# Kernel optimization log

Hardware: AMD Instinct MI355X
Metric: run time of the kernel (lower is better)

The kernel has to match this reference:

```python
import jax, jax.numpy as jnp
import numpy as np

OUTPUT_SIZE = 512


def _build_schedule(n, m):
    """Static pyramid-circuit schedule of Givens/RBS gates on n wires.

    Sequential gate order (matches theta ordering): for k = 1..n-1, apply
    gates on adjacent wire pairs (i, i+1) for i = k-1 down to max(k-m, 0).
    Total gates = (2n - m - 1) * m // 2. Gates are packed into a brickwork
    schedule (timestep t = 2(k-1) - i) so each layer touches disjoint pairs
    and the whole chain runs in T = n + m - 2 parallel layers.
    Padded slots point at dummy wires (n, n+1) and are masked to identity.
    """
    layers = {}
    t_idx = 0
    for k in range(1, n):
        for i in range(k - 1, max(k - m, 0) - 1, -1):
            t = 2 * (k - 1) - i
            layers.setdefault(t, []).append((i, t_idx))
            t_idx += 1
    T = max(layers) + 1
    W = max(len(v) for v in layers.values())
    wire = np.full((T, W), n, dtype=np.int32)   # pad gates hit dummy wires (n, n+1)
    tidx = np.zeros((T, W), dtype=np.int32)
    mask = np.zeros((T, W), dtype=np.float32)
    for t, gs in layers.items():
        for j, (i, ti) in enumerate(gs):
            wire[t, j] = i
            tidx[t, j] = ti
            mask[t, j] = 1.0
    return wire, tidx, mask


def apply_orthogonal(thetas, x, output_size):
    input_size = x.shape[-1]
    n, m = max(input_size, output_size), min(input_size, output_size)
    wire, tidx, mask = _build_schedule(n, m)
    if input_size < n:
        x = jnp.pad(x, ((0, 0), (0, n - input_size)))
    state = jnp.pad(x, ((0, 0), (0, 2)))          # two dummy columns for padded gate slots
    th = thetas[jnp.asarray(tidx)]                # [T, W]
    msk = jnp.asarray(mask)
    cos = jnp.where(msk > 0, jnp.cos(th), 1.0)    # padded slots -> identity rotation
    sin = jnp.where(msk > 0, jnp.sin(th), 0.0)
    wa = jnp.asarray(wire)                        # [T, W] first wire of each pair
    wb = wa + 1

    def step(st, layer):
        c, s, a_idx, b_idx = layer
        a = st[:, a_idx]                          # [B, W]
        b = st[:, b_idx]
        st = st.at[:, a_idx].set(c * a + s * b)   # RBS rotation on each pair
        st = st.at[:, b_idx].set(c * b - s * a)
        return st, None

    state, _ = jax.lax.scan(step, state, (cos, sin, wa, wb))
    return state[:, :output_size]


def setup_inputs():
    key = jax.random.key(0)
    k1, k2 = jax.random.split(key)
    B, N = 256, 512
    n_thetas = (2 * max(N, OUTPUT_SIZE) - min(N, OUTPUT_SIZE) - 1) * min(N, OUTPUT_SIZE) // 2
    x = jax.random.normal(k1, (B, N), dtype=jnp.float32)
    thetas = jax.random.uniform(k2, (n_thetas,), dtype=jnp.float32,
                                minval=-np.pi, maxval=np.pi)
    bias = jnp.zeros((OUTPUT_SIZE,), dtype=jnp.float32)
    return {"x": x, "thetas": thetas, "bias": bias}


def reference(x, thetas, bias):
    # normalize_inputs=False path; with_bias=True
    out = apply_orthogonal(thetas, x, OUTPUT_SIZE)
    return out + bias
```

## Files before the change

kernel.cpp:

```cpp
#include <hip/hip_runtime.h>
#include <stdint.h>


#define N_WIRES 512
#define BATCH   256
#define PAIRS   510
#define HALFP   255
#define PF      5
#define FINAL4  (PAIRS * 256)
#define TOTAL4  (FINAL4 + 128)
#define TOTAL2  (TOTAL4 * 2)

__global__ __launch_bounds__(256) void fused_kernel(
    const float* __restrict__ thetas, float2* __restrict__ W2) {
  int tid = blockIdx.x * 256 + threadIdx.x;
  if (tid >= TOTAL2) return;
  float c = 1.0f, s = 0.0f;
  if (tid < PAIRS * 512) {
    int p = tid >> 9, r = tid & 511;
    int q = r >> 7, L = (r >> 1) & 63, e = r & 1, h = q >> 1;
    int t = 2 * p + h;
    int i = 8 * L + 4 * (q & 1) + 2 * e + h;
    if (i <= min(t, 1020 - t)) {
      int k = ((t + i) >> 1) + 1;
      int idx = ((k * (k - 1)) >> 1) + (k - 1 - i);
      __sincosf(thetas[idx], &s, &c);
    }
    if (q == 3 && e == 1) c -= 1.0f;
  } else {
    int e = tid - PAIRS * 512;
    int L = e >> 2, j = e & 3;
    if (8 * L + 2 * j == 0) __sincosf(thetas[130815], &s, &c);
  }
  W2[tid] = make_float2(c, s);
}

template <int N>
__device__ __forceinline__ void wait_vm() {
  asm volatile("s_waitcnt vmcnt(%0)" ::"i"(N) : "memory");
}

__device__ __forceinline__ float dpp_shr1(float v) {
  return __int_as_float(
      __builtin_amdgcn_mov_dpp(__float_as_int(v), 0x138, 0xF, 0xF, true));
}
__device__ __forceinline__ float dpp_shl1(float v) {
  return __int_as_float(
      __builtin_amdgcn_mov_dpp(__float_as_int(v), 0x130, 0xF, 0xF, true));
}

__device__ __forceinline__ void gate_pk2(float2 cs, float2& ab) {
  float2 t;
  asm("v_pk_mul_f32 %0, %1, %2 op_sel:[1,1] op_sel_hi:[1,0] neg_hi:[1,0]"
      : "=v"(t)
      : "v"(cs), "v"(ab));
  asm("v_pk_fma_f32 %0, %1, %0, %2 op_sel:[0,0,0] op_sel_hi:[0,1,1]"
      : "+v"(ab)
      : "v"(cs), "v"(t));
}

__device__ __forceinline__ void gate_s(float& a, float& b, float c, float s) {
  float na = fmaf(c, a, s * b);
  float nb = fmaf(c, b, -(s * a));
  a = na;
  b = nb;
}

__device__ __forceinline__ void pair_compute(float2& A, float2& B, float2& C,
                                             float2& D, const float4& q0,
                                             const float4& q1, const float4& q2,
                                             const float4& q3) {
  gate_pk2(make_float2(q0.x, q0.y), A);
  gate_pk2(make_float2(q0.z, q0.w), B);
  gate_pk2(make_float2(q1.x, q1.y), C);
  gate_pk2(make_float2(q1.z, q1.w), D);
  float cl_m1 = dpp_shr1(q3.z);
  float sl    = dpp_shr1(q3.w);
  float rv0 = dpp_shl1(A.x);
  float lv7 = dpp_shr1(D.y);
  gate_s(A.y, B.x, q2.x, q2.y);
  gate_s(B.y, C.x, q2.z, q2.w);
  gate_s(C.y, D.x, q3.x, q3.y);
  float nv7 = fmaf(q3.w, rv0, fmaf(q3.z, D.y, D.y));
  float nv0 = fmaf(-sl, lv7, fmaf(cl_m1, A.x, A.x));
  D.y = nv7;
  A.x = nv0;
}

__device__ __forceinline__ void run_255(const float4* __restrict__ Wg, int p0,
                                        int lane, float2& A, float2& B,
                                        float2& C, float2& D) {
  const float4* pb = Wg + p0 * 256;
  float4 R[PF][4];
#pragma unroll
  for (int s = 0; s < PF; ++s) {
    R[s][0] = pb[lane];
    R[s][1] = pb[64 + lane];
    R[s][2] = pb[128 + lane];
    R[s][3] = pb[192 + lane];
    pb += 256;
  }
  for (int blk = 0; blk < 50; ++blk) {
#pragma unroll
    for (int s = 0; s < PF; ++s) {
      wait_vm<16>();
      pair_compute(A, B, C, D, R[s][0], R[s][1], R[s][2], R[s][3]);
      R[s][0] = pb[lane];
      R[s][1] = pb[64 + lane];
      R[s][2] = pb[128 + lane];
      R[s][3] = pb[192 + lane];
      pb += 256;
    }
  }
  wait_vm<0>();
#pragma unroll
  for (int s = 0; s < PF; ++s)
    pair_compute(A, B, C, D, R[s][0], R[s][1], R[s][2], R[s][3]);
}

__global__ __launch_bounds__(64, 1) void phase_kernel(
    const float* __restrict__ x, const float* __restrict__ W,
    float* __restrict__ T1, float* __restrict__ ML) {
  const int lane = threadIdx.x;
  const int b = blockIdx.x;
  const bool late = (b >= BATCH);
  const float4* __restrict__ Wg = (const float4*)W;

  float2 A, B, C, D;
  if (!late) {
    const float4* xr = (const float4*)(x + b * N_WIRES) + lane * 2;
    float4 x0 = xr[0], x1 = xr[1];
    A = make_float2(x0.x, x0.y); B = make_float2(x0.z, x0.w);
    C = make_float2(x1.x, x1.y); D = make_float2(x1.z, x1.w);
    run_255(Wg, 0, lane, A, B, C, D);
    float* tr = T1 + b * N_WIRES + lane * 8;
    *(float4*)tr = make_float4(A.x, A.y, B.x, B.y);
    *(float4*)(tr + 4) = make_float4(C.x, C.y, D.x, D.y);
  } else {
    const int u = b - BATCH;
    const int base = lane * 8;
    A = make_float2(base + 0 == u ? 1.f : 0.f, base + 1 == u ? 1.f : 0.f);
    B = make_float2(base + 2 == u ? 1.f : 0.f, base + 3 == u ? 1.f : 0.f);
    C = make_float2(base + 4 == u ? 1.f : 0.f, base + 5 == u ? 1.f : 0.f);
    D = make_float2(base + 6 == u ? 1.f : 0.f, base + 7 == u ? 1.f : 0.f);
    run_255(Wg, HALFP, lane, A, B, C, D);
    float4 f0 = Wg[FINAL4 + lane];
    float4 f1 = Wg[FINAL4 + 64 + lane];
    gate_pk2(make_float2(f0.x, f0.y), A);
    gate_pk2(make_float2(f0.z, f0.w), B);
    gate_pk2(make_float2(f1.x, f1.y), C);
    gate_pk2(make_float2(f1.z, f1.w), D);
    float* mr = ML + u * N_WIRES + lane * 8;
    *(float4*)mr = make_float4(A.x, A.y, B.x, B.y);
    *(float4*)(mr + 4) = make_float4(C.x, C.y, D.x, D.y);
  }
}

__global__ __launch_bounds__(256) void gemm_kernel(
    const float* __restrict__ T1, const float* __restrict__ ML,
    const float* __restrict__ bias, float* __restrict__ out) {
  __shared__ float a_s[1024];
  const int tid = threadIdx.x;
  const int half = tid >> 7, j = tid & 127;
  const int rbase = blockIdx.x * 2;
  for (int i = tid; i < 1024; i += 256) a_s[i] = T1[rbase * N_WIRES + i];
  __syncthreads();
  const float4* __restrict__ ML4 = (const float4*)ML;
  float4 acc = make_float4(0.f, 0.f, 0.f, 0.f);
#pragma unroll 8
  for (int u = 0; u < 512; ++u) {
    float a = a_s[half * 512 + u];
    float4 m = ML4[u * 128 + j];
    acc.x = fmaf(a, m.x, acc.x);
    acc.y = fmaf(a, m.y, acc.y);
    acc.z = fmaf(a, m.z, acc.z);
    acc.w = fmaf(a, m.w, acc.w);
  }
  float4 bv = ((const float4*)bias)[j];
  acc.x += bv.x; acc.y += bv.y; acc.z += bv.z; acc.w += bv.w;
  ((float4*)out)[(rbase + half) * 128 + j] = acc;
}

__global__ __launch_bounds__(64, 1) void circuit_full(
    const float* __restrict__ x, const float* __restrict__ W,
    const float* __restrict__ bias, float* __restrict__ out) {
  const int lane = threadIdx.x;
  const int row = blockIdx.x;
  const float4* __restrict__ Wg = (const float4*)W;

  const float4* pb = Wg;
  float4 R[PF][4];
#pragma unroll
  for (int s = 0; s < PF; ++s) {
    R[s][0] = pb[lane]; R[s][1] = pb[64 + lane];
    R[s][2] = pb[128 + lane]; R[s][3] = pb[192 + lane];
    pb += 256;
  }
  const float4* xr = (const float4*)(x + row * N_WIRES) + lane * 2;
  float4 x0 = xr[0], x1 = xr[1];
  float2 A = make_float2(x0.x, x0.y), B = make_float2(x0.z, x0.w);
  float2 C = make_float2(x1.x, x1.y), D = make_float2(x1.z, x1.w);

  for (int blk = 0; blk < 101; ++blk) {
#pragma unroll
    for (int s = 0; s < PF; ++s) {
      wait_vm<16>();
      pair_compute(A, B, C, D, R[s][0], R[s][1], R[s][2], R[s][3]);
      R[s][0] = pb[lane]; R[s][1] = pb[64 + lane];
      R[s][2] = pb[128 + lane]; R[s][3] = pb[192 + lane];
      pb += 256;
    }
  }
  wait_vm<0>();
#pragma unroll
  for (int s = 0; s < PF; ++s)
    pair_compute(A, B, C, D, R[s][0], R[s][1], R[s][2], R[s][3]);

  float4 f0 = Wg[FINAL4 + lane];
  float4 f1 = Wg[FINAL4 + 64 + lane];
  gate_pk2(make_float2(f0.x, f0.y), A);
  gate_pk2(make_float2(f0.z, f0.w), B);
  gate_pk2(make_float2(f1.x, f1.y), C);
  gate_pk2(make_float2(f1.z, f1.w), D);

  const float* br = bias + lane * 8;
  float4 b0 = *(const float4*)(br);
  float4 b1 = *(const float4*)(br + 4);
  float* orow = out + row * N_WIRES + lane * 8;
  *(float4*)(orow) = make_float4(A.x + b0.x, A.y + b0.y, B.x + b0.z, B.y + b0.w);
  *(float4*)(orow + 4) = make_float4(C.x + b1.x, C.y + b1.y, D.x + b1.z, D.y + b1.w);
}

extern "C" void kernel_launch(void* const* d_in, const int* in_sizes, int n_in,
                              void* d_out, int out_size, void* d_ws,
                              size_t ws_size, hipStream_t stream) {
  const float* x = (const float*)d_in[0];
  const float* thetas = (const float*)d_in[1];
  const float* bias = (const float*)d_in[2];
  float* out = (float*)d_out;

  float* W = (float*)d_ws;
  const size_t table_bytes = (size_t)TOTAL4 * 16;
  const size_t t1_bytes = (size_t)BATCH * N_WIRES * 4;
  const size_t ml_bytes = (size_t)N_WIRES * N_WIRES * 4;

  fused_kernel<<<TOTAL2 / 256, 256, 0, stream>>>(thetas, (float2*)W);

  if (ws_size >= table_bytes + t1_bytes + ml_bytes) {
    float* T1 = (float*)((char*)d_ws + table_bytes);
    float* ML = T1 + BATCH * N_WIRES;
    phase_kernel<<<BATCH + N_WIRES, 64, 0, stream>>>(x, W, T1, ML);
    gemm_kernel<<<BATCH / 2, 256, 0, stream>>>(T1, ML, bias, out);
  } else {
    circuit_full<<<BATCH, 64, 0, stream>>>(x, W, bias, out);
  }
}
```

Before: 126.0 us.

## Share gate-table loads across four waves via LDS triple buffering; split GEMM reduction

The phase kernel now runs four rows per 256-thread block. The rotation table is streamed into LDS in chunks with global_load_lds into three rotating buffers, so the four waves share one global fetch per chunk instead of each wave streaming the whole table from global or L2. The last three pair-steps are preloaded into registers. The GEMM uses one row per block and splits the K dimension across two thread halves, reducing through shared memory, which doubles the number of blocks. This adds per-chunk __syncthreads barriers on the serial dependent circuit chain, and the blocks may become latency-bound on LDS reads.

New measurement: 120.2 us. 4.6% less time.

```diff
diff --git a/kernel.cpp b/kernel.cpp
--- a/kernel.cpp
+++ b/kernel.cpp
@@ -5,8 +5,10 @@
 #define N_WIRES 512
 #define BATCH   256
 #define PAIRS   510
-#define HALFP   255
-#define PF      5
+#define SEGP    255
+#define CH      4
+#define NCH     63
+#define CH4     (CH * 256)
 #define FINAL4  (PAIRS * 256)
 #define TOTAL4  (FINAL4 + 128)
 #define TOTAL2  (TOTAL4 * 2)
@@ -87,69 +89,104 @@
   A.x = nv0;
 }
 
-__device__ __forceinline__ void run_255(const float4* __restrict__ Wg, int p0,
-                                        int lane, float2& A, float2& B,
-                                        float2& C, float2& D) {
-  const float4* pb = Wg + p0 * 256;
-  float4 R[PF][4];
-#pragma unroll
-  for (int s = 0; s < PF; ++s) {
-    R[s][0] = pb[lane];
-    R[s][1] = pb[64 + lane];
-    R[s][2] = pb[128 + lane];
-    R[s][3] = pb[192 + lane];
-    pb += 256;
-  }
-  for (int blk = 0; blk < 50; ++blk) {
-#pragma unroll
-    for (int s = 0; s < PF; ++s) {
-      wait_vm<16>();
-      pair_compute(A, B, C, D, R[s][0], R[s][1], R[s][2], R[s][3]);
-      R[s][0] = pb[lane];
-      R[s][1] = pb[64 + lane];
-      R[s][2] = pb[128 + lane];
-      R[s][3] = pb[192 + lane];
-      pb += 256;
-    }
-  }
-  wait_vm<0>();
-#pragma unroll
-  for (int s = 0; s < PF; ++s)
-    pair_compute(A, B, C, D, R[s][0], R[s][1], R[s][2], R[s][3]);
-}
-
-__global__ __launch_bounds__(64, 1) void phase_kernel(
+__device__ __forceinline__ void issue_chunk(const float4* __restrict__ seg,
+                                            float4* smem, int c, int bi,
+                                            int wave, int lane) {
+  const float4* src = seg + c * CH4 + wave * 4 * 64 + lane;
+  float4* dst = smem + bi * CH4 + wave * 4 * 64;
+#pragma unroll
+  for (int j = 0; j < 4; ++j) {
+    __builtin_amdgcn_global_load_lds(
+        (__attribute__((address_space(1))) uint32_t*)(src + j * 64),
+        (__attribute__((address_space(3))) uint32_t*)(dst + j * 64),
+        16, 0, 0);
+  }
+}
+
+__global__ __launch_bounds__(256, 1) void phase_kernel(
     const float* __restrict__ x, const float* __restrict__ W,
     float* __restrict__ T1, float* __restrict__ ML) {
-  const int lane = threadIdx.x;
+  __shared__ float4 smem[3 * CH4];
+  const int lane = threadIdx.x & 63;
+  const int wave = threadIdx.x >> 6;
   const int b = blockIdx.x;
-  const bool late = (b >= BATCH);
+  const bool late = b >= (BATCH / 4);
   const float4* __restrict__ Wg = (const float4*)W;
+  const float4* seg = Wg + (late ? SEGP : 0) * 256;
+
+  float4 Tl[3][4];
+#pragma unroll
+  for (int pr = 0; pr < 3; ++pr) {
+    const float4* pb = seg + (252 + pr) * 256;
+#pragma unroll
+    for (int q = 0; q < 4; ++q) Tl[pr][q] = pb[q * 64 + lane];
+  }
+  issue_chunk(seg, smem, 0, 0, wave, lane);
+  issue_chunk(seg, smem, 1, 1, wave, lane);
 
   float2 A, B, C, D;
   if (!late) {
-    const float4* xr = (const float4*)(x + b * N_WIRES) + lane * 2;
+    const int row = b * 4 + wave;
+    const float4* xr = (const float4*)(x + row * N_WIRES) + lane * 2;
     float4 x0 = xr[0], x1 = xr[1];
     A = make_float2(x0.x, x0.y); B = make_float2(x0.z, x0.w);
     C = make_float2(x1.x, x1.y); D = make_float2(x1.z, x1.w);
-    run_255(Wg, 0, lane, A, B, C, D);
-    float* tr = T1 + b * N_WIRES + lane * 8;
-    *(float4*)tr = make_float4(A.x, A.y, B.x, B.y);
-    *(float4*)(tr + 4) = make_float4(C.x, C.y, D.x, D.y);
   } else {
-    const int u = b - BATCH;
+    const int u = (b - BATCH / 4) * 4 + wave;
     const int base = lane * 8;
     A = make_float2(base + 0 == u ? 1.f : 0.f, base + 1 == u ? 1.f : 0.f);
     B = make_float2(base + 2 == u ? 1.f : 0.f, base + 3 == u ? 1.f : 0.f);
     C = make_float2(base + 4 == u ? 1.f : 0.f, base + 5 == u ? 1.f : 0.f);
     D = make_float2(base + 6 == u ? 1.f : 0.f, base + 7 == u ? 1.f : 0.f);
-    run_255(Wg, HALFP, lane, A, B, C, D);
+  }
+
+  int bsel = 0;
+  for (int k = 0; k < NCH - 1; ++k) {
+    wait_vm<4>();
+    __syncthreads();
+    const float4* buf = smem + bsel * CH4;
+#pragma unroll
+    for (int pr = 0; pr < CH; ++pr) {
+      pair_compute(A, B, C, D, buf[(pr * 4 + 0) * 64 + lane],
+                   buf[(pr * 4 + 1) * 64 + lane],
+                   buf[(pr * 4 + 2) * 64 + lane],
+                   buf[(pr * 4 + 3) * 64 + lane]);
+    }
+    if (k + 2 < NCH) {
+      int nb = bsel + 2; if (nb >= 3) nb -= 3;
+      issue_chunk(seg, smem, k + 2, nb, wave, lane);
+    }
+    bsel = (bsel == 2) ? 0 : bsel + 1;
+  }
+  wait_vm<0>();
+  __syncthreads();
+  {
+    const float4* buf = smem + bsel * CH4;
+#pragma unroll
+    for (int pr = 0; pr < CH; ++pr) {
+      pair_compute(A, B, C, D, buf[(pr * 4 + 0) * 64 + lane],
+                   buf[(pr * 4 + 1) * 64 + lane],
+                   buf[(pr * 4 + 2) * 64 + lane],
+                   buf[(pr * 4 + 3) * 64 + lane]);
+    }
+  }
+#pragma unroll
+  for (int pr = 0; pr < 3; ++pr)
+    pair_compute(A, B, C, D, Tl[pr][0], Tl[pr][1], Tl[pr][2], Tl[pr][3]);
+
+  if (!late) {
+    const int row = b * 4 + wave;
+    float* tr = T1 + row * N_WIRES + lane * 8;
+    *(float4*)tr = make_float4(A.x, A.y, B.x, B.y);
+    *(float4*)(tr + 4) = make_float4(C.x, C.y, D.x, D.y);
+  } else {
     float4 f0 = Wg[FINAL4 + lane];
     float4 f1 = Wg[FINAL4 + 64 + lane];
     gate_pk2(make_float2(f0.x, f0.y), A);
     gate_pk2(make_float2(f0.z, f0.w), B);
     gate_pk2(make_float2(f1.x, f1.y), C);
     gate_pk2(make_float2(f1.z, f1.w), D);
+    const int u = (b - BATCH / 4) * 4 + wave;
     float* mr = ML + u * N_WIRES + lane * 8;
     *(float4*)mr = make_float4(A.x, A.y, B.x, B.y);
     *(float4*)(mr + 4) = make_float4(C.x, C.y, D.x, D.y);
@@ -159,28 +196,38 @@
 __global__ __launch_bounds__(256) void gemm_kernel(
     const float* __restrict__ T1, const float* __restrict__ ML,
     const float* __restrict__ bias, float* __restrict__ out) {
-  __shared__ float a_s[1024];
+  __shared__ float a_s[512];
+  __shared__ float4 part[128];
   const int tid = threadIdx.x;
-  const int half = tid >> 7, j = tid & 127;
-  const int rbase = blockIdx.x * 2;
-  for (int i = tid; i < 1024; i += 256) a_s[i] = T1[rbase * N_WIRES + i];
+  const int j = tid & 127, uh = tid >> 7;
+  const int row = blockIdx.x;
+  a_s[tid] = T1[row * N_WIRES + tid];
+  a_s[tid + 256] = T1[row * N_WIRES + tid + 256];
   __syncthreads();
   const float4* __restrict__ ML4 = (const float4*)ML;
   float4 acc = make_float4(0.f, 0.f, 0.f, 0.f);
+  const int u0 = uh * 256;
 #pragma unroll 8
-  for (int u = 0; u < 512; ++u) {
-    float a = a_s[half * 512 + u];
-    float4 m = ML4[u * 128 + j];
+  for (int du = 0; du < 256; ++du) {
+    float a = a_s[u0 + du];
+    float4 m = ML4[(u0 + du) * 128 + j];
     acc.x = fmaf(a, m.x, acc.x);
     acc.y = fmaf(a, m.y, acc.y);
     acc.z = fmaf(a, m.z, acc.z);
     acc.w = fmaf(a, m.w, acc.w);
   }
-  float4 bv = ((const float4*)bias)[j];
-  acc.x += bv.x; acc.y += bv.y; acc.z += bv.z; acc.w += bv.w;
-  ((float4*)out)[(rbase + half) * 128 + j] = acc;
-}
-
+  if (uh == 1) part[j] = acc;
+  __syncthreads();
+  if (uh == 0) {
+    float4 p = part[j];
+    float4 bv = ((const float4*)bias)[j];
+    acc.x += p.x + bv.x; acc.y += p.y + bv.y;
+    acc.z += p.z + bv.z; acc.w += p.w + bv.w;
+    ((float4*)out)[row * 128 + j] = acc;
+  }
+}
+
+#define PF 5
 __global__ __launch_bounds__(64, 1) void circuit_full(
     const float* __restrict__ x, const float* __restrict__ W,
     const float* __restrict__ bias, float* __restrict__ out) {
@@ -249,8 +296,8 @@
   if (ws_size >= table_bytes + t1_bytes + ml_bytes) {
     float* T1 = (float*)((char*)d_ws + table_bytes);
     float* ML = T1 + BATCH * N_WIRES;
-    phase_kernel<<<BATCH + N_WIRES, 64, 0, stream>>>(x, W, T1, ML);
-    gemm_kernel<<<BATCH / 2, 256, 0, stream>>>(T1, ML, bias, out);
+    phase_kernel<<<BATCH / 4 + N_WIRES / 4, 256, 0, stream>>>(x, W, T1, ML);
+    gemm_kernel<<<BATCH, 256, 0, stream>>>(T1, ML, bias, out);
   } else {
     circuit_full<<<BATCH, 64, 0, stream>>>(x, W, bias, out);
   }
```
